# Performance work log

Hardware: AMD Instinct MI355X
Metric: run time of the kernel (lower is better)

## Reference

```python
import jax, jax.numpy as jnp
import numpy as np

B, L, D, H = 4, 1024, 1024, 16
HD = D // H
EPS = 1e-5


def _split_heads(x):
    b, l, d = x.shape
    return x.reshape(b, l, H, HD).transpose(0, 2, 1, 3)  # [B,H,L,hd]


def _combine_heads(x):
    b, h, l, hd = x.shape
    return x.transpose(0, 2, 1, 3).reshape(b, l, h * hd)


def _attention(q, k, v):
    scores = jnp.einsum('bhqd,bhkd->bhqk', q, k) / jnp.sqrt(jnp.asarray(HD, q.dtype))
    w = jax.nn.softmax(scores, axis=-1)  # dropout is identity in eval mode
    return jnp.einsum('bhqk,bhkd->bhqd', w, v)


def _layernorm(x, g, b):
    mu = jnp.mean(x, axis=-1, keepdims=True)
    var = jnp.mean(jnp.square(x - mu), axis=-1, keepdims=True)
    return (x - mu) * jax.lax.rsqrt(var + EPS) * g + b


def setup_inputs() -> dict:
    key = jax.random.key(0)
    ks = jax.random.split(key, 20)
    s = 1.0 / np.sqrt(D)
    s2 = 1.0 / np.sqrt(2 * D)
    # weights stored as (in, out): y = x @ W + b
    inp = {
        'h_b': jax.random.normal(ks[0], (B, L, D), jnp.float32),
        'h_p': jax.random.normal(ks[1], (B, L, D), jnp.float32),
        'wq': jax.random.uniform(ks[2], (D, D), jnp.float32, -s, s),
        'bq': jnp.zeros((D,), jnp.float32),
        'wk_sem': jax.random.uniform(ks[3], (D, D), jnp.float32, -s, s),
        'bk_sem': jnp.zeros((D,), jnp.float32),
        'wk_syn': jax.random.uniform(ks[4], (D, D), jnp.float32, -s, s),
        'bk_syn': jnp.zeros((D,), jnp.float32),
        'wv': jax.random.uniform(ks[5], (D, D), jnp.float32, -s, s),
        'bv': jnp.zeros((D,), jnp.float32),
        'g_sem_w': jax.random.uniform(ks[6], (2 * D, D), jnp.float32, -s2, s2),
        'g_sem_b': jnp.zeros((D,), jnp.float32),
        'g_syn_w': jax.random.uniform(ks[7], (2 * D, D), jnp.float32, -s2, s2),
        'g_syn_b': jnp.zeros((D,), jnp.float32),
        'ln_sem_g': jnp.ones((D,), jnp.float32),
        'ln_sem_b': jnp.zeros((D,), jnp.float32),
        'ln_syn_g': jnp.ones((D,), jnp.float32),
        'ln_syn_b': jnp.zeros((D,), jnp.float32),
        'fg1_w': jax.random.uniform(ks[8], (2 * D, D), jnp.float32, -s2, s2),
        'fg1_b': jnp.zeros((D,), jnp.float32),
        'fg2_w': jax.random.uniform(ks[9], (D, 1), jnp.float32, -s, s),
        'fg2_b': jnp.zeros((1,), jnp.float32),
    }
    return inp


def reference(h_b, h_p, wq, bq, wk_sem, bk_sem, wk_syn, bk_syn, wv, bv,
              g_sem_w, g_sem_b, g_syn_w, g_syn_b,
              ln_sem_g, ln_sem_b, ln_syn_g, ln_syn_b,
              fg1_w, fg1_b, fg2_w, fg2_b):
    def cross_attn(a, b, kw, kb):
        q = _split_heads(a @ wq + bq)
        k = _split_heads(b @ kw + kb)
        v = _split_heads(b @ wv + bv)
        return _combine_heads(_attention(q, k, v))

    def gate_fusion(orig, enh, gw, gb):
        gate = jax.nn.sigmoid(jnp.concatenate([orig, enh], axis=-1) @ gw + gb)
        return gate * enh + (1.0 - gate) * orig

    # semantic branch: query=h_b, kv=h_p with syntax K/V projections
    enh_b = cross_attn(h_b, h_p, wk_syn, bk_syn)
    hbp = gate_fusion(h_b, enh_b, g_sem_w, g_sem_b)
    hbp = _layernorm(hbp + h_b, ln_sem_g, ln_sem_b)

    # syntax branch: query=h_p, kv=h_b with semantic K projection (as in source)
    enh_p = cross_attn(h_p, h_b, wk_sem, bk_sem)
    hpp = gate_fusion(h_p, enh_p, g_syn_w, g_syn_b)
    hpp = _layernorm(hpp + h_p, ln_syn_g, ln_syn_b)

    cat = jnp.concatenate([hbp, hpp], axis=-1)
    fw = jax.nn.sigmoid(jax.nn.relu(cat @ fg1_w + fg1_b) @ fg2_w + fg2_b)  # [B,L,1]
    return fw * hbp + (1.0 - fw) * hpp
```

## Files before the change

### kernel.cpp

```cpp
#include <hip/hip_runtime.h>


typedef __bf16 bf16;
typedef __attribute__((ext_vector_type(4))) __bf16 bf16x4;
typedef __attribute__((ext_vector_type(8))) __bf16 bf16x8;
typedef __attribute__((ext_vector_type(4))) float f32x4;

#define MFMA16(a, b, c) __builtin_amdgcn_mfma_f32_16x16x32_bf16((a), (b), (c), 0, 0, 0)
#define EXP2(x) __builtin_amdgcn_exp2f(x)

__device__ inline void async16(const bf16* g, bf16* l) {
  __builtin_amdgcn_global_load_lds(
      (const __attribute__((address_space(1))) unsigned int*)g,
      (__attribute__((address_space(3))) unsigned int*)l, 16, 0, 0);
}

__global__ __launch_bounds__(256) void prep_k(
    const float* __restrict__ wq, const float* __restrict__ wk_sem,
    const float* __restrict__ wk_syn, const float* __restrict__ wv,
    const float* __restrict__ g_sem_w, const float* __restrict__ g_syn_w,
    const float* __restrict__ fg1_w, bf16* __restrict__ wqT,
    bf16* __restrict__ wkSemT, bf16* __restrict__ wkSynT,
    bf16* __restrict__ wvT, bf16* __restrict__ gSemT,
    bf16* __restrict__ gSynT, bf16* __restrict__ fg1T) {
  __shared__ bf16 t[32][33];
  int blk = blockIdx.x, tid = threadIdx.x;
  const float* in;
  bf16* out;
  int R, tile;
  if (blk < 4096) {
    int which = blk >> 10;
    tile = blk & 1023;
    R = 1024;
    in = (which == 0) ? wq : (which == 1) ? wk_sem : (which == 2) ? wk_syn : wv;
    out = (which == 0) ? wqT
          : (which == 1) ? wkSemT : (which == 2) ? wkSynT : wvT;
  } else {
    int b2 = blk - 4096;
    int which = b2 >> 11;
    tile = b2 & 2047;
    R = 2048;
    in = (which == 0) ? g_sem_w : (which == 1) ? g_syn_w : fg1_w;
    out = (which == 0) ? gSemT : (which == 1) ? gSynT : fg1T;
  }
  const int C = 1024;
  int c0 = (tile & 31) * 32, r0 = (tile >> 5) * 32;
  int tx = tid & 31, ty = tid >> 5;
#pragma unroll
  for (int i = 0; i < 32; i += 8)
    t[ty + i][tx] = (bf16)in[(size_t)(r0 + ty + i) * C + c0 + tx];
  __syncthreads();
#pragma unroll
  for (int i = 0; i < 32; i += 8)
    out[(size_t)(c0 + ty + i) * R + r0 + tx] = t[tx][ty + i];
}

__device__ inline void stageA_f32(bf16* As, const float* Asrc, int m0, int tid) {
#pragma unroll
  for (int i = 0; i < 2; i++) {
    int s = tid + i * 256;
    int row = s >> 2, ch = s & 3;
    const float* p = Asrc + (size_t)(m0 + row) * 1024 + ch * 8;
    f32x4 x = *(const f32x4*)p, y = *(const f32x4*)(p + 4);
    bf16x8 r;
#pragma unroll
    for (int j = 0; j < 4; j++) { r[j] = (bf16)x[j]; r[4 + j] = (bf16)y[j]; }
    *(bf16x8*)(As + s * 8) = r;
  }
}
__device__ inline void stageA_bf16(bf16* As, const bf16* Asrc, int m0, int tid) {
#pragma unroll
  for (int i = 0; i < 2; i++) {
    int s = tid + i * 256;
    int row = s >> 2, ch = s & 3;
    async16(Asrc + (size_t)(m0 + row) * 1024 + ch * 8,
            As + ((size_t)(i * 256 + (tid & ~63))) * 8);
  }
}
__device__ inline void stageB(bf16* Bs, const bf16* Wt, int n0, int k0, int ldk,
                              int tid) {
#pragma unroll
  for (int i = 0; i < 2; i++) {
    int s = tid + i * 256;
    int row = s >> 2, ch = s & 3;
    async16(Wt + (size_t)(n0 + row) * ldk + k0 + ch * 8,
            Bs + ((size_t)(i * 256 + (tid & ~63))) * 8);
  }
}

__global__ __launch_bounds__(256) void proj_gemm(
    const float* __restrict__ h_b, const float* __restrict__ h_p,
    const bf16* __restrict__ wqT, const bf16* __restrict__ wkSemT,
    const bf16* __restrict__ wkSynT, const bf16* __restrict__ wvT,
    const float* __restrict__ bq, const float* __restrict__ bk_sem,
    const float* __restrict__ bk_syn, const float* __restrict__ bv,
    bf16* __restrict__ q0, bf16* __restrict__ q1, bf16* __restrict__ k0b,
    bf16* __restrict__ k1b, bf16* __restrict__ v0t, bf16* __restrict__ v1t) {
  __shared__ bf16 As[128 * 32];
  __shared__ bf16 Bs[128 * 32];
  int tid = threadIdx.x;
  int m0g = blockIdx.y * 128;
  int half = m0g >= 4096;
  int m0 = m0g & 4095;
  int n0g = blockIdx.x * 128;
  int seg = n0g >> 10, n0 = n0g & 1023;

  const float* A = half ? h_p : h_b;
  const bf16* Wt = (seg == 0) ? wqT
                   : (seg == 1) ? (half ? wkSynT : wkSemT) : wvT;
  const float* bias = (seg == 0) ? bq
                      : (seg == 1) ? (half ? bk_syn : bk_sem) : bv;

  int w = tid >> 6, lane = tid & 63, quad = lane >> 4, ln = lane & 15;
  int wm = (w >> 1) * 64, wn = (w & 1) * 64;

  const f32x4 z = {0.f, 0.f, 0.f, 0.f};
  f32x4 acc[4][4];
#pragma unroll
  for (int i = 0; i < 4; i++)
#pragma unroll
    for (int j = 0; j < 4; j++) acc[i][j] = z;

  for (int k0 = 0; k0 < 1024; k0 += 32) {
    __syncthreads();
    stageB(Bs, Wt, n0, k0, 1024, tid);
    stageA_f32(As, A + k0, m0, tid);
    __syncthreads();
    bf16x8 af[4], bfv[4];
#pragma unroll
    for (int mt = 0; mt < 4; mt++)
      af[mt] = *(bf16x8*)(As + (wm + mt * 16 + ln) * 32 + quad * 8);
#pragma unroll
    for (int nt = 0; nt < 4; nt++)
      bfv[nt] = *(bf16x8*)(Bs + (wn + nt * 16 + ln) * 32 + quad * 8);
#pragma unroll
    for (int mt = 0; mt < 4; mt++)
#pragma unroll
      for (int nt = 0; nt < 4; nt++)
        acc[mt][nt] = MFMA16(af[mt], bfv[nt], acc[mt][nt]);
  }

  if (seg == 2) {
    bf16* vt = half ? v0t : v1t;
#pragma unroll
    for (int nt = 0; nt < 4; nt++) {
      int n = n0 + wn + nt * 16 + ln;
      float bvv = bias[n];
#pragma unroll
      for (int mt = 0; mt < 4; mt++) {
        int mb = m0 + wm + mt * 16 + quad * 4;
        bf16x4 pk;
#pragma unroll
        for (int r = 0; r < 4; r++) pk[r] = (bf16)(acc[mt][nt][r] + bvv);
        *(bf16x4*)(vt + (size_t)n * 4096 + mb) = pk;
      }
    }
    return;
  }
  const float scale = (seg == 0) ? 0.1803368801f : 1.f;
  bf16* out = (seg == 0) ? (half ? q1 : q0) : (half ? k0b : k1b);
#pragma unroll
  for (int nt = 0; nt < 4; nt++) {
    int n = n0 + wn + nt * 16 + ln;
    float bvv = bias[n];
#pragma unroll
    for (int mt = 0; mt < 4; mt++) {
      int mb = m0 + wm + mt * 16 + quad * 4;
#pragma unroll
      for (int r = 0; r < 4; r++)
        out[(size_t)(mb + r) * 1024 + n] =
            (bf16)((acc[mt][nt][r] + bvv) * scale);
    }
  }
}

__global__ __launch_bounds__(256) void gate_gemm(
    const float* __restrict__ h_b, const float* __restrict__ h_p,
    const bf16* __restrict__ e0, const bf16* __restrict__ e1,
    const bf16* __restrict__ gSemT, const bf16* __restrict__ gSynT,
    const float* __restrict__ g_sem_b, const float* __restrict__ g_syn_b,
    bf16* __restrict__ ln0, bf16* __restrict__ ln1) {
  __shared__ bf16 As[128 * 32];
  __shared__ bf16 Bs[128 * 32];
  int tid = threadIdx.x;
  int m0g = blockIdx.y * 128;
  int half = m0g >= 4096;
  int m0 = m0g & 4095;
  int n0 = blockIdx.x * 128;

  const float* A0 = half ? h_p : h_b;
  const bf16* A1 = half ? e1 : e0;
  const bf16* Wt = half ? gSynT : gSemT;
  const float* bias = half ? g_syn_b : g_sem_b;
  bf16* out = half ? ln1 : ln0;

  int w = tid >> 6, lane = tid & 63, quad = lane >> 4, ln = lane & 15;
  int wm = (w >> 1) * 64, wn = (w & 1) * 64;

  const f32x4 z = {0.f, 0.f, 0.f, 0.f};
  f32x4 acc[4][4];
#pragma unroll
  for (int i = 0; i < 4; i++)
#pragma unroll
    for (int j = 0; j < 4; j++) acc[i][j] = z;

  for (int k0 = 0; k0 < 2048; k0 += 32) {
    __syncthreads();
    stageB(Bs, Wt, n0, k0, 2048, tid);
    if (k0 < 1024)
      stageA_f32(As, A0 + k0, m0, tid);
    else
      stageA_bf16(As, A1 + (k0 - 1024), m0, tid);
    __syncthreads();
    bf16x8 af[4], bfv[4];
#pragma unroll
    for (int mt = 0; mt < 4; mt++)
      af[mt] = *(bf16x8*)(As + (wm + mt * 16 + ln) * 32 + quad * 8);
#pragma unroll
    for (int nt = 0; nt < 4; nt++)
      bfv[nt] = *(bf16x8*)(Bs + (wn + nt * 16 + ln) * 32 + quad * 8);
#pragma unroll
    for (int mt = 0; mt < 4; mt++)
#pragma unroll
      for (int nt = 0; nt < 4; nt++)
        acc[mt][nt] = MFMA16(af[mt], bfv[nt], acc[mt][nt]);
  }

#pragma unroll
  for (int nt = 0; nt < 4; nt++) {
    int n = n0 + wn + nt * 16 + ln;
    float bvv = bias[n];
#pragma unroll
    for (int mt = 0; mt < 4; mt++) {
      int mb = m0 + wm + mt * 16 + quad * 4;
#pragma unroll
      for (int r = 0; r < 4; r++) {
        size_t idx = (size_t)(mb + r) * 1024 + n;
        float v = acc[mt][nt][r] + bvv;
        float e = (float)A1[idx], o = A0[idx];
        float g = 1.f / (1.f + __expf(-v));
        out[idx] = (bf16)(g * e + (1.f - g) * o + o);
      }
    }
  }
}

__global__ __launch_bounds__(256) void fg1_gemm(
    const bf16* __restrict__ A0, const bf16* __restrict__ A1,
    const bf16* __restrict__ Wt, const float* __restrict__ bias,
    bf16* __restrict__ out) {
  __shared__ bf16 As[128 * 32];
  __shared__ bf16 Bs[128 * 32];
  int tid = threadIdx.x;
  int m0 = blockIdx.y * 128, n0 = blockIdx.x * 128;
  int w = tid >> 6, lane = tid & 63, quad = lane >> 4, ln = lane & 15;
  int wm = (w >> 1) * 64, wn = (w & 1) * 64;

  const f32x4 z = {0.f, 0.f, 0.f, 0.f};
  f32x4 acc[4][4];
#pragma unroll
  for (int i = 0; i < 4; i++)
#pragma unroll
    for (int j = 0; j < 4; j++) acc[i][j] = z;

  for (int k0 = 0; k0 < 2048; k0 += 32) {
    __syncthreads();
    stageB(Bs, Wt, n0, k0, 2048, tid);
    if (k0 < 1024)
      stageA_bf16(As, A0 + k0, m0, tid);
    else
      stageA_bf16(As, A1 + (k0 - 1024), m0, tid);
    __syncthreads();
    bf16x8 af[4], bfv[4];
#pragma unroll
    for (int mt = 0; mt < 4; mt++)
      af[mt] = *(bf16x8*)(As + (wm + mt * 16 + ln) * 32 + quad * 8);
#pragma unroll
    for (int nt = 0; nt < 4; nt++)
      bfv[nt] = *(bf16x8*)(Bs + (wn + nt * 16 + ln) * 32 + quad * 8);
#pragma unroll
    for (int mt = 0; mt < 4; mt++)
#pragma unroll
      for (int nt = 0; nt < 4; nt++)
        acc[mt][nt] = MFMA16(af[mt], bfv[nt], acc[mt][nt]);
  }

#pragma unroll
  for (int nt = 0; nt < 4; nt++) {
    int n = n0 + wn + nt * 16 + ln;
    float bvv = bias[n];
#pragma unroll
    for (int mt = 0; mt < 4; mt++) {
      int mb = m0 + wm + mt * 16 + quad * 4;
#pragma unroll
      for (int r = 0; r < 4; r++)
        out[(size_t)(mb + r) * 1024 + n] =
            (bf16)fmaxf(acc[mt][nt][r] + bvv, 0.f);
    }
  }
}

__global__ __launch_bounds__(256) void attn_k(
    const bf16* __restrict__ q0, const bf16* __restrict__ q1,
    const bf16* __restrict__ k0b, const bf16* __restrict__ k1b,
    const bf16* __restrict__ v0t, const bf16* __restrict__ v1t,
    bf16* __restrict__ e0, bf16* __restrict__ e1) {
  int x = blockIdx.x;
  int branch = (x >> 3) & 1;
  int bh = (x & 7) * 8 + ((x >> 4) & 7);
  int qblk = x >> 7;
  int h = bh & 15, b = bh >> 4;
  const bf16* Q = branch ? q1 : q0;
  const bf16* Kp = branch ? k1b : k0b;
  const bf16* Vg = branch ? v1t : v0t;
  bf16* O = branch ? e1 : e0;
  size_t kbase = ((size_t)b * 1024) * 1024 + h * 64;
  size_t vbase = (size_t)h * 64 * 4096 + b * 1024;

  __shared__ bf16 Kt[2 * 64 * 32];
  __shared__ bf16 Vt[2 * 64 * 32];
  __shared__ bf16 Pw[4][2 * 16 * 32];

  int tid = threadIdx.x, w = tid >> 6, lane = tid & 63;
  int quad = lane >> 4, ln = lane & 15;
  int wq0 = qblk * 64 + w * 16;

  bf16x8 qf0 = *(const bf16x8*)(Q + kbase + (size_t)(wq0 + ln) * 1024 + quad * 8);
  bf16x8 qf1 =
      *(const bf16x8*)(Q + kbase + (size_t)(wq0 + ln) * 1024 + 32 + quad * 8);

  const f32x4 z = {0.f, 0.f, 0.f, 0.f};
  f32x4 oacc[4];
#pragma unroll
  for (int i = 0; i < 4; i++) oacc[i] = z;
  float m_run = -1e30f, l_run = 0.f;

  for (int kv0 = 0; kv0 < 1024; kv0 += 64) {
    __syncthreads();
#pragma unroll
    for (int i = 0; i < 2; i++) {
      int s = tid + i * 256;
      size_t wb = (size_t)(i * 256 + (tid & ~63)) * 8;
      async16(Kp + kbase + (size_t)(kv0 + ((s >> 2) & 63)) * 1024 +
                  (s >> 8) * 32 + (s & 3) * 8,
              Kt + wb);
      async16(Vg + vbase + (size_t)((s >> 2) & 63) * 4096 + kv0 +
                  (s >> 8) * 32 + (s & 3) * 8,
              Vt + wb);
    }
    __syncthreads();

    f32x4 s[4];
#pragma unroll
    for (int nt = 0; nt < 4; nt++) {
      bf16x8 kf0 = *(bf16x8*)(Kt + (nt * 16 + ln) * 32 + quad * 8);
      bf16x8 kf1 = *(bf16x8*)(Kt + 2048 + (nt * 16 + ln) * 32 + quad * 8);
      f32x4 a = z;
      a = MFMA16(kf0, qf0, a);
      a = MFMA16(kf1, qf1, a);
      s[nt] = a;
    }

    float mx = s[0][0];
#pragma unroll
    for (int nt = 0; nt < 4; nt++)
#pragma unroll
      for (int r = 0; r < 4; r++) mx = fmaxf(mx, s[nt][r]);
    mx = fmaxf(mx, __shfl_xor(mx, 16, 64));
    mx = fmaxf(mx, __shfl_xor(mx, 32, 64));

    float mn = fmaxf(m_run, mx);
    float alpha = EXP2(m_run - mn);
    m_run = mn;

    float rs = 0.f;
#pragma unroll
    for (int nt = 0; nt < 4; nt++)
#pragma unroll
      for (int r = 0; r < 4; r++) {
        float p = EXP2(s[nt][r] - mn);
        s[nt][r] = p;
        rs += p;
      }
    rs += __shfl_xor(rs, 16, 64);
    rs += __shfl_xor(rs, 32, 64);
    l_run = l_run * alpha + rs;

    float a_r[4];
#pragma unroll
    for (int r = 0; r < 4; r++) a_r[r] = __shfl(alpha, quad * 4 + r, 16);
#pragma unroll
    for (int dt = 0; dt < 4; dt++)
#pragma unroll
      for (int r = 0; r < 4; r++) oacc[dt][r] *= a_r[r];

#pragma unroll
    for (int nt = 0; nt < 4; nt++) {
      bf16x4 pk;
#pragma unroll
      for (int r = 0; r < 4; r++) pk[r] = (bf16)s[nt][r];
      *(bf16x4*)(Pw[w] + (nt >> 1) * 512 + ln * 32 + (nt & 1) * 16 + quad * 4) =
          pk;
    }

    bf16x8 pa0 = *(bf16x8*)(Pw[w] + ln * 32 + quad * 8);
    bf16x8 pa1 = *(bf16x8*)(Pw[w] + 512 + ln * 32 + quad * 8);
#pragma unroll
    for (int dt = 0; dt < 4; dt++) {
      bf16x8 vb0 = *(bf16x8*)(Vt + (dt * 16 + ln) * 32 + quad * 8);
      bf16x8 vb1 = *(bf16x8*)(Vt + 2048 + (dt * 16 + ln) * 32 + quad * 8);
      oacc[dt] = MFMA16(pa0, vb0, oacc[dt]);
      oacc[dt] = MFMA16(pa1, vb1, oacc[dt]);
    }
  }

  float l_r[4];
#pragma unroll
  for (int r = 0; r < 4; r++)
    l_r[r] = 1.f / __shfl(l_run, quad * 4 + r, 16);
#pragma unroll
  for (int dt = 0; dt < 4; dt++)
#pragma unroll
    for (int r = 0; r < 4; r++) {
      int q = wq0 + quad * 4 + r;
      O[kbase + (size_t)q * 1024 + dt * 16 + ln] =
          (bf16)(oacc[dt][r] * l_r[r]);
    }
}

__global__ __launch_bounds__(256) void ln_k(
    const bf16* __restrict__ x0, const bf16* __restrict__ x1,
    const float* __restrict__ g0, const float* __restrict__ b0,
    const float* __restrict__ g1, const float* __restrict__ b1,
    bf16* __restrict__ y0, bf16* __restrict__ y1) {
  int rowg = blockIdx.x, tid = threadIdx.x, c = tid * 4;
  int half = rowg >= 4096;
  int row = rowg & 4095;
  const bf16* x = half ? x1 : x0;
  const float* gg = half ? g1 : g0;
  const float* bb = half ? b1 : b0;
  bf16* y = half ? y1 : y0;

  bf16x4 x4 = *(const bf16x4*)(x + (size_t)row * 1024 + c);
  float v[4], s = 0.f, ss = 0.f;
#pragma unroll
  for (int i = 0; i < 4; i++) {
    v[i] = (float)x4[i];
    s += v[i];
    ss += v[i] * v[i];
  }
#pragma unroll
  for (int o = 32; o > 0; o >>= 1) {
    s += __shfl_down(s, o, 64);
    ss += __shfl_down(ss, o, 64);
  }
  __shared__ float red[8];
  int w = tid >> 6;
  if ((tid & 63) == 0) { red[w] = s; red[4 + w] = ss; }
  __syncthreads();
  s = red[0] + red[1] + red[2] + red[3];
  ss = red[4] + red[5] + red[6] + red[7];
  float mu = s * (1.f / 1024.f);
  float var = ss * (1.f / 1024.f) - mu * mu;
  float rstd = rsqrtf(var + 1e-5f);
  f32x4 g4 = *(const f32x4*)(gg + c), b4 = *(const f32x4*)(bb + c);
  bf16x4 o4;
#pragma unroll
  for (int i = 0; i < 4; i++) o4[i] = (bf16)((v[i] - mu) * rstd * g4[i] + b4[i]);
  *(bf16x4*)(y + (size_t)row * 1024 + c) = o4;
}

__global__ __launch_bounds__(256) void fg2mix_k(const bf16* __restrict__ t,
                                                const float* __restrict__ w2,
                                                const float* __restrict__ b2,
                                                const bf16* __restrict__ hbp,
                                                const bf16* __restrict__ hpp,
                                                float* __restrict__ out) {
  int row = blockIdx.x, tid = threadIdx.x, c = tid * 4;
  bf16x4 t4 = *(const bf16x4*)(t + (size_t)row * 1024 + c);
  f32x4 w4 = *(const f32x4*)(w2 + c);
  float s = 0.f;
#pragma unroll
  for (int i = 0; i < 4; i++) s += (float)t4[i] * w4[i];
#pragma unroll
  for (int o = 32; o > 0; o >>= 1) s += __shfl_down(s, o, 64);
  __shared__ float red[4];
  if ((tid & 63) == 0) red[tid >> 6] = s;
  __syncthreads();
  s = red[0] + red[1] + red[2] + red[3];
  float fw = 1.f / (1.f + __expf(-(s + b2[0])));
  bf16x4 a4 = *(const bf16x4*)(hbp + (size_t)row * 1024 + c);
  bf16x4 p4 = *(const bf16x4*)(hpp + (size_t)row * 1024 + c);
  f32x4 o4;
#pragma unroll
  for (int i = 0; i < 4; i++)
    o4[i] = fw * (float)a4[i] + (1.f - fw) * (float)p4[i];
  *(f32x4*)(out + (size_t)row * 1024 + c) = o4;
}

extern "C" void kernel_launch(void* const* d_in, const int* in_sizes, int n_in,
                              void* d_out, int out_size, void* d_ws,
                              size_t ws_size, hipStream_t stream) {
  const float* h_b     = (const float*)d_in[0];
  const float* h_p     = (const float*)d_in[1];
  const float* wq      = (const float*)d_in[2];
  const float* bq      = (const float*)d_in[3];
  const float* wk_sem  = (const float*)d_in[4];
  const float* bk_sem  = (const float*)d_in[5];
  const float* wk_syn  = (const float*)d_in[6];
  const float* bk_syn  = (const float*)d_in[7];
  const float* wv      = (const float*)d_in[8];
  const float* bv      = (const float*)d_in[9];
  const float* g_sem_w = (const float*)d_in[10];
  const float* g_sem_b = (const float*)d_in[11];
  const float* g_syn_w = (const float*)d_in[12];
  const float* g_syn_b = (const float*)d_in[13];
  const float* ln_sem_g = (const float*)d_in[14];
  const float* ln_sem_b = (const float*)d_in[15];
  const float* ln_syn_g = (const float*)d_in[16];
  const float* ln_syn_b = (const float*)d_in[17];
  const float* fg1_w   = (const float*)d_in[18];
  const float* fg1_b   = (const float*)d_in[19];
  const float* fg2_w   = (const float*)d_in[20];
  const float* fg2_b   = (const float*)d_in[21];

  bf16* ws = (bf16*)d_ws;
  const size_t M1 = 1024ull * 1024ull;
  bf16* wqT    = ws + 0 * M1;
  bf16* wkSemT = ws + 1 * M1;
  bf16* wkSynT = ws + 2 * M1;
  bf16* wvT    = ws + 3 * M1;
  bf16* gSemT  = ws + 4 * M1;
  bf16* gSynT  = ws + 6 * M1;
  bf16* fg1T   = ws + 8 * M1;
  bf16* q0  = ws + 10 * M1;
  bf16* q1  = ws + 14 * M1;
  bf16* k0b = ws + 18 * M1;
  bf16* k1b = ws + 22 * M1;
  bf16* v0t = ws + 26 * M1;
  bf16* v1t = ws + 30 * M1;
  bf16* e0b = ws + 34 * M1;
  bf16* e1b = ws + 38 * M1;
  bf16* ln0 = q0;
  bf16* ln1 = q1;
  bf16* hbp = k0b;
  bf16* hpp = k1b;
  bf16* tb  = v0t;

  prep_k<<<10240, 256, 0, stream>>>(wq, wk_sem, wk_syn, wv, g_sem_w, g_syn_w,
                                    fg1_w, wqT, wkSemT, wkSynT, wvT, gSemT,
                                    gSynT, fg1T);

  proj_gemm<<<dim3(24, 64), 256, 0, stream>>>(
      h_b, h_p, wqT, wkSemT, wkSynT, wvT, bq, bk_sem, bk_syn, bv,
      q0, q1, k0b, k1b, v0t, v1t);

  attn_k<<<2048, 256, 0, stream>>>(q0, q1, k0b, k1b, v0t, v1t, e0b, e1b);

  gate_gemm<<<dim3(8, 64), 256, 0, stream>>>(
      h_b, h_p, e0b, e1b, gSemT, gSynT, g_sem_b, g_syn_b, ln0, ln1);

  ln_k<<<8192, 256, 0, stream>>>(ln0, ln1, ln_sem_g, ln_sem_b, ln_syn_g,
                                 ln_syn_b, hbp, hpp);

  fg1_gemm<<<dim3(8, 32), 256, 0, stream>>>(hbp, hpp, fg1T, fg1_b, tb);

  fg2mix_k<<<4096, 256, 0, stream>>>(tb, fg2_w, fg2_b, hbp, hpp,
                                     (float*)d_out);
}
```

Baseline: 461.0 us.

## Pre-convert inputs to bf16 for async LDS staging; shrink fg1 GEMM M-tile

The prep kernel now also converts h_b and h_p to bf16, writing them into the output buffer as scratch. The projection and gate GEMMs can then stage their A operand with async global-to-LDS loads instead of fp32 loads followed by register conversion. The fg1 GEMM tile drops from 128 to 64 rows, doubling its grid for better occupancy. This adds an extra conversion pass and relies on d_out being free until the final kernel overwrites it.

```diff
diff --git a/kernel.cpp b/kernel.cpp
--- a/kernel.cpp
+++ b/kernel.cpp
@@ -19,12 +19,26 @@
     const float* __restrict__ wq, const float* __restrict__ wk_sem,
     const float* __restrict__ wk_syn, const float* __restrict__ wv,
     const float* __restrict__ g_sem_w, const float* __restrict__ g_syn_w,
-    const float* __restrict__ fg1_w, bf16* __restrict__ wqT,
+    const float* __restrict__ fg1_w, const float* __restrict__ h_b,
+    const float* __restrict__ h_p, bf16* __restrict__ wqT,
     bf16* __restrict__ wkSemT, bf16* __restrict__ wkSynT,
     bf16* __restrict__ wvT, bf16* __restrict__ gSemT,
-    bf16* __restrict__ gSynT, bf16* __restrict__ fg1T) {
+    bf16* __restrict__ gSynT, bf16* __restrict__ fg1T,
+    bf16* __restrict__ hbb, bf16* __restrict__ hpb) {
+  int blk = blockIdx.x, tid = threadIdx.x;
+  if (blk >= 10240) {
+    int idx = blk - 10240;
+    const float* in = (idx < 2048) ? h_b : h_p;
+    bf16* out = (idx < 2048) ? hbb : hpb;
+    size_t base = (size_t)(idx & 2047) * 2048 + tid * 8;
+    f32x4 x = *(const f32x4*)(in + base), y = *(const f32x4*)(in + base + 4);
+    bf16x8 r;
+#pragma unroll
+    for (int j = 0; j < 4; j++) { r[j] = (bf16)x[j]; r[4 + j] = (bf16)y[j]; }
+    *(bf16x8*)(out + base) = r;
+    return;
+  }
   __shared__ bf16 t[32][33];
-  int blk = blockIdx.x, tid = threadIdx.x;
   const float* in;
   bf16* out;
   int R, tile;
@@ -55,41 +69,25 @@
     out[(size_t)(c0 + ty + i) * R + r0 + tx] = t[tx][ty + i];
 }
 
-__device__ inline void stageA_f32(bf16* As, const float* Asrc, int m0, int tid) {
+__device__ inline void stage128(bf16* Ls, const bf16* src, int r0, int k0,
+                                int ldk, int tid) {
 #pragma unroll
   for (int i = 0; i < 2; i++) {
     int s = tid + i * 256;
     int row = s >> 2, ch = s & 3;
-    const float* p = Asrc + (size_t)(m0 + row) * 1024 + ch * 8;
-    f32x4 x = *(const f32x4*)p, y = *(const f32x4*)(p + 4);
-    bf16x8 r;
-#pragma unroll
-    for (int j = 0; j < 4; j++) { r[j] = (bf16)x[j]; r[4 + j] = (bf16)y[j]; }
-    *(bf16x8*)(As + s * 8) = r;
-  }
-}
-__device__ inline void stageA_bf16(bf16* As, const bf16* Asrc, int m0, int tid) {
-#pragma unroll
-  for (int i = 0; i < 2; i++) {
-    int s = tid + i * 256;
-    int row = s >> 2, ch = s & 3;
-    async16(Asrc + (size_t)(m0 + row) * 1024 + ch * 8,
-            As + ((size_t)(i * 256 + (tid & ~63))) * 8);
-  }
-}
-__device__ inline void stageB(bf16* Bs, const bf16* Wt, int n0, int k0, int ldk,
-                              int tid) {
-#pragma unroll
-  for (int i = 0; i < 2; i++) {
-    int s = tid + i * 256;
-    int row = s >> 2, ch = s & 3;
-    async16(Wt + (size_t)(n0 + row) * ldk + k0 + ch * 8,
-            Bs + ((size_t)(i * 256 + (tid & ~63))) * 8);
-  }
+    async16(src + (size_t)(r0 + row) * ldk + k0 + ch * 8,
+            Ls + ((size_t)(i * 256 + (tid & ~63))) * 8);
+  }
+}
+__device__ inline void stage64(bf16* Ls, const bf16* src, int r0, int k0,
+                               int ldk, int tid) {
+  int row = tid >> 2, ch = tid & 3;
+  async16(src + (size_t)(r0 + row) * ldk + k0 + ch * 8,
+          Ls + ((size_t)(tid & ~63)) * 8);
 }
 
 __global__ __launch_bounds__(256) void proj_gemm(
-    const float* __restrict__ h_b, const float* __restrict__ h_p,
+    const bf16* __restrict__ hbb, const bf16* __restrict__ hpb,
     const bf16* __restrict__ wqT, const bf16* __restrict__ wkSemT,
     const bf16* __restrict__ wkSynT, const bf16* __restrict__ wvT,
     const float* __restrict__ bq, const float* __restrict__ bk_sem,
@@ -105,7 +103,7 @@
   int n0g = blockIdx.x * 128;
   int seg = n0g >> 10, n0 = n0g & 1023;
 
-  const float* A = half ? h_p : h_b;
+  const bf16* A = half ? hpb : hbb;
   const bf16* Wt = (seg == 0) ? wqT
                    : (seg == 1) ? (half ? wkSynT : wkSemT) : wvT;
   const float* bias = (seg == 0) ? bq
@@ -123,8 +121,8 @@
 
   for (int k0 = 0; k0 < 1024; k0 += 32) {
     __syncthreads();
-    stageB(Bs, Wt, n0, k0, 1024, tid);
-    stageA_f32(As, A + k0, m0, tid);
+    stage128(Bs, Wt, n0, k0, 1024, tid);
+    stage128(As, A, m0, k0, 1024, tid);
     __syncthreads();
     bf16x8 af[4], bfv[4];
 #pragma unroll
@@ -175,6 +173,7 @@
 }
 
 __global__ __launch_bounds__(256) void gate_gemm(
+    const bf16* __restrict__ hbb, const bf16* __restrict__ hpb,
     const float* __restrict__ h_b, const float* __restrict__ h_p,
     const bf16* __restrict__ e0, const bf16* __restrict__ e1,
     const bf16* __restrict__ gSemT, const bf16* __restrict__ gSynT,
@@ -188,7 +187,8 @@
   int m0 = m0g & 4095;
   int n0 = blockIdx.x * 128;
 
-  const float* A0 = half ? h_p : h_b;
+  const bf16* A0 = half ? hpb : hbb;
+  const float* O0 = half ? h_p : h_b;
   const bf16* A1 = half ? e1 : e0;
   const bf16* Wt = half ? gSynT : gSemT;
   const float* bias = half ? g_syn_b : g_sem_b;
@@ -206,11 +206,11 @@
 
   for (int k0 = 0; k0 < 2048; k0 += 32) {
     __syncthreads();
-    stageB(Bs, Wt, n0, k0, 2048, tid);
+    stage128(Bs, Wt, n0, k0, 2048, tid);
     if (k0 < 1024)
-      stageA_f32(As, A0 + k0, m0, tid);
+      stage128(As, A0, m0, k0, 1024, tid);
     else
-      stageA_bf16(As, A1 + (k0 - 1024), m0, tid);
+      stage128(As, A1, m0, k0 - 1024, 1024, tid);
     __syncthreads();
     bf16x8 af[4], bfv[4];
 #pragma unroll
@@ -237,7 +237,7 @@
       for (int r = 0; r < 4; r++) {
         size_t idx = (size_t)(mb + r) * 1024 + n;
         float v = acc[mt][nt][r] + bvv;
-        float e = (float)A1[idx], o = A0[idx];
+        float e = (float)A1[idx], o = O0[idx];
         float g = 1.f / (1.f + __expf(-v));
         out[idx] = (bf16)(g * e + (1.f - g) * o + o);
       }
@@ -249,37 +249,37 @@
     const bf16* __restrict__ A0, const bf16* __restrict__ A1,
     const bf16* __restrict__ Wt, const float* __restrict__ bias,
     bf16* __restrict__ out) {
-  __shared__ bf16 As[128 * 32];
+  __shared__ bf16 As[64 * 32];
   __shared__ bf16 Bs[128 * 32];
   int tid = threadIdx.x;
-  int m0 = blockIdx.y * 128, n0 = blockIdx.x * 128;
+  int m0 = blockIdx.y * 64, n0 = blockIdx.x * 128;
   int w = tid >> 6, lane = tid & 63, quad = lane >> 4, ln = lane & 15;
-  int wm = (w >> 1) * 64, wn = (w & 1) * 64;
+  int wm = (w >> 1) * 32, wn = (w & 1) * 64;
 
   const f32x4 z = {0.f, 0.f, 0.f, 0.f};
-  f32x4 acc[4][4];
-#pragma unroll
-  for (int i = 0; i < 4; i++)
+  f32x4 acc[2][4];
+#pragma unroll
+  for (int i = 0; i < 2; i++)
 #pragma unroll
     for (int j = 0; j < 4; j++) acc[i][j] = z;
 
   for (int k0 = 0; k0 < 2048; k0 += 32) {
     __syncthreads();
-    stageB(Bs, Wt, n0, k0, 2048, tid);
+    stage128(Bs, Wt, n0, k0, 2048, tid);
     if (k0 < 1024)
-      stageA_bf16(As, A0 + k0, m0, tid);
+      stage64(As, A0, m0, k0, 1024, tid);
     else
-      stageA_bf16(As, A1 + (k0 - 1024), m0, tid);
-    __syncthreads();
-    bf16x8 af[4], bfv[4];
-#pragma unroll
-    for (int mt = 0; mt < 4; mt++)
+      stage64(As, A1, m0, k0 - 1024, 1024, tid);
+    __syncthreads();
+    bf16x8 af[2], bfv[4];
+#pragma unroll
+    for (int mt = 0; mt < 2; mt++)
       af[mt] = *(bf16x8*)(As + (wm + mt * 16 + ln) * 32 + quad * 8);
 #pragma unroll
     for (int nt = 0; nt < 4; nt++)
       bfv[nt] = *(bf16x8*)(Bs + (wn + nt * 16 + ln) * 32 + quad * 8);
 #pragma unroll
-    for (int mt = 0; mt < 4; mt++)
+    for (int mt = 0; mt < 2; mt++)
 #pragma unroll
       for (int nt = 0; nt < 4; nt++)
         acc[mt][nt] = MFMA16(af[mt], bfv[nt], acc[mt][nt]);
@@ -290,7 +290,7 @@
     int n = n0 + wn + nt * 16 + ln;
     float bvv = bias[n];
 #pragma unroll
-    for (int mt = 0; mt < 4; mt++) {
+    for (int mt = 0; mt < 2; mt++) {
       int mb = m0 + wm + mt * 16 + quad * 4;
 #pragma unroll
       for (int r = 0; r < 4; r++)
@@ -511,8 +511,8 @@
   const float* bk_syn  = (const float*)d_in[7];
   const float* wv      = (const float*)d_in[8];
   const float* bv      = (const float*)d_in[9];
+  const float* g_sem_b = (const float*)d_in[11];
   const float* g_sem_w = (const float*)d_in[10];
-  const float* g_sem_b = (const float*)d_in[11];
   const float* g_syn_w = (const float*)d_in[12];
   const float* g_syn_b = (const float*)d_in[13];
   const float* ln_sem_g = (const float*)d_in[14];
@@ -541,29 +541,31 @@
   bf16* v1t = ws + 30 * M1;
   bf16* e0b = ws + 34 * M1;
   bf16* e1b = ws + 38 * M1;
+  bf16* hbb = (bf16*)d_out;
+  bf16* hpb = hbb + 4 * M1;
   bf16* ln0 = q0;
   bf16* ln1 = q1;
   bf16* hbp = k0b;
   bf16* hpp = k1b;
   bf16* tb  = v0t;
 
-  prep_k<<<10240, 256, 0, stream>>>(wq, wk_sem, wk_syn, wv, g_sem_w, g_syn_w,
-                                    fg1_w, wqT, wkSemT, wkSynT, wvT, gSemT,
-                                    gSynT, fg1T);
+  prep_k<<<14336, 256, 0, stream>>>(wq, wk_sem, wk_syn, wv, g_sem_w, g_syn_w,
+                                    fg1_w, h_b, h_p, wqT, wkSemT, wkSynT, wvT,
+                                    gSemT, gSynT, fg1T, hbb, hpb);
 
   proj_gemm<<<dim3(24, 64), 256, 0, stream>>>(
-      h_b, h_p, wqT, wkSemT, wkSynT, wvT, bq, bk_sem, bk_syn, bv,
+      hbb, hpb, wqT, wkSemT, wkSynT, wvT, bq, bk_sem, bk_syn, bv,
       q0, q1, k0b, k1b, v0t, v1t);
 
   attn_k<<<2048, 256, 0, stream>>>(q0, q1, k0b, k1b, v0t, v1t, e0b, e1b);
 
   gate_gemm<<<dim3(8, 64), 256, 0, stream>>>(
-      h_b, h_p, e0b, e1b, gSemT, gSynT, g_sem_b, g_syn_b, ln0, ln1);
+      hbb, hpb, h_b, h_p, e0b, e1b, gSemT, gSynT, g_sem_b, g_syn_b, ln0, ln1);
 
   ln_k<<<8192, 256, 0, stream>>>(ln0, ln1, ln_sem_g, ln_sem_b, ln_syn_g,
                                  ln_syn_b, hbp, hpp);
 
-  fg1_gemm<<<dim3(8, 32), 256, 0, stream>>>(hbp, hpp, fg1T, fg1_b, tb);
+  fg1_gemm<<<dim3(8, 64), 256, 0, stream>>>(hbp, hpp, fg1T, fg1_b, tb);
 
   fg2mix_k<<<4096, 256, 0, stream>>>(tb, fg2_w, fg2_b, hbp, hpp,
                                      (float*)d_out);
```

New measurement: 418.3 us. 1.1x faster.
